# Optimization experiments

Hardware: AMD Instinct MI355X
Metric: run time of the kernel (lower is better)

## Reference

```python
import jax, jax.numpy as jnp
import numpy as np
import math

S, B, D_MODEL = 1024, 2, 1024
N_HEADS = 16
D_HEAD = D_MODEL // N_HEADS
C = 32  # compressed_len


def _xavier(key, shape):
    fan_in, fan_out = shape[-1], shape[-2] if len(shape) > 1 else shape[-1]
    limit = math.sqrt(6.0 / (fan_in + fan_out))
    return jax.random.uniform(key, shape, jnp.float32, -limit, limit)


def setup_inputs() -> dict:
    key = jax.random.key(0)
    ks = jax.random.split(key, 10)
    return {
        "x": jax.random.normal(ks[0], (S, B, D_MODEL), jnp.float32),
        "q_down": _xavier(ks[1], (C, D_MODEL)),
        "Wq": _xavier(ks[2], (D_MODEL, D_MODEL)),
        "bq": jnp.zeros((D_MODEL,), jnp.float32),
        "Wk": _xavier(ks[3], (D_MODEL, D_MODEL)),
        "bk": jnp.zeros((D_MODEL,), jnp.float32),
        "Wv": _xavier(ks[4], (D_MODEL, D_MODEL)),
        "bv": jnp.zeros((D_MODEL,), jnp.float32),
        "Wo": _xavier(ks[5], (D_MODEL, D_MODEL)),
        "bo": jnp.zeros((D_MODEL,), jnp.float32),
    }


def reference(x, q_down, Wq, bq, Wk, bk, Wv, bv, Wo, bo):
    # x: (s, b, d_model); causal=True, rope=None, dropout inactive (eval)
    s, b, d_model = x.shape
    h, dh = N_HEADS, D_HEAD
    scale = 1.0 / math.sqrt(dh)

    q_u = x @ Wq.T + bq                       # (s,b,dm)
    k_d = x @ Wk.T + bk
    v_d = x @ Wv.T + bv
    v_d_k = v_d @ Wk.T + bk
    v_d_v = v_d @ Wv.T + bv

    def heads(t):  # (s,b,dm) -> (b,h,s,dh)
        return t.reshape(s, b, h, dh).transpose(1, 2, 0, 3)

    q_u = heads(q_u) * scale
    k_d = heads(k_d)
    v_d_kv = jnp.concatenate([heads(v_d_k), heads(v_d_v)], axis=-1)  # (b,h,s,2dh)

    q_d = q_down.reshape(C, h, dh).transpose(1, 0, 2) * scale        # (h,c,dh)

    down = jnp.einsum('hcd,bhsd->bhcs', q_d, k_d)                    # (b,h,c,s)
    w = jnp.exp(down - jnp.max(down, axis=-1, keepdims=True))
    norm = jnp.cumsum(w, axis=-1)

    # (b,h,c,s,2dh): running compressed KV state
    kv_u = jnp.cumsum(w[..., None] * v_d_kv[:, :, None, :, :], axis=3) / norm[..., None]
    k_u, v_u = jnp.split(kv_u, 2, axis=-1)                           # each (b,h,c,s,dh)

    up = jnp.einsum('bhsd,bhcsd->bhsc', q_u, k_u)
    up = jax.nn.softmax(up, axis=-1)
    out = jnp.einsum('bhsc,bhcsd->bhsd', up, v_u)                    # (b,h,s,dh)

    out = out.transpose(2, 0, 1, 3).reshape(s, b, d_model)
    return out @ Wo.T + bo
```

## Files before the change

### kernel.cpp

```cpp
#include <hip/hip_runtime.h>
#include <cstdint>
#include <cstddef>

#define S_LEN 1024
#define BATCH 2
#define DM    1024
#define NH    16
#define DH    64
#define CC    32
#define SB    2048
#define TSD   128
#define NCHD  8

using short8 = __attribute__((ext_vector_type(8))) short;
using f32x4  = __attribute__((ext_vector_type(4))) float;

__device__ __forceinline__ float b2f(unsigned short u) {
    union { unsigned int i; float f; } v; v.i = ((unsigned int)u) << 16; return v.f;
}
__device__ __forceinline__ unsigned short f2b(float f) {
    union { float f; unsigned int i; } v; v.f = f;
    unsigned int x = v.i;
    unsigned int r = x + 0x7FFFu + ((x >> 16) & 1u);
    return (unsigned short)(r >> 16);
}

__device__ __forceinline__ void async_ld16(const unsigned short* g, unsigned short* l) {
    __builtin_amdgcn_global_load_lds(
        (const __attribute__((address_space(1))) unsigned int*)g,
        (__attribute__((address_space(3))) unsigned int*)l,
        16, 0, 0);
}

__global__ __launch_bounds__(256) void k_convert(
    const void* x, const void* qd,
    const void* wq, const void* wk, const void* wv, const void* wo,
    const void* bq, const void* bk, const void* bv, const void* bo,
    int* __restrict__ flag,
    unsigned short* xb, unsigned short* qdb,
    unsigned short* Wqb, unsigned short* Wkb, unsigned short* Wvb, unsigned short* Wob,
    float* biasf)
{
    __shared__ int cnt;
    if (threadIdx.x == 0) cnt = 0;
    __syncthreads();
    {
        const unsigned short* xs = (const unsigned short*)x;
        int local = 0;
        for (int i = threadIdx.x; i < 1024; i += 256) {
            unsigned e = (xs[i * 2] >> 7) & 0xFF;
            if (e >= 90 && e <= 160) local++;
        }
        atomicAdd(&cnt, local);
    }
    __syncthreads();
    const int isbf = (cnt >= 640);
    if (blockIdx.x == 0 && threadIdx.x == 0) *flag = isbf;

    const size_t tid = (size_t)blockIdx.x * 256 + threadIdx.x;
    const size_t stride = (size_t)gridDim.x * 256;

    if (!isbf) {
        auto cv = [&](const void* src, unsigned short* dst, size_t n) {
            const float4* s = (const float4*)src;
            for (size_t i = tid; i < n / 4; i += stride) {
                float4 v = s[i];
                ushort4 o;
                o.x = f2b(v.x); o.y = f2b(v.y); o.z = f2b(v.z); o.w = f2b(v.w);
                ((ushort4*)dst)[i] = o;
            }
        };
        cv(x,  xb,  (size_t)SB * DM);
        cv(qd, qdb, (size_t)CC * DM);
        cv(wq, Wqb, (size_t)DM * DM);
        cv(wk, Wkb, (size_t)DM * DM);
        cv(wv, Wvb, (size_t)DM * DM);
        cv(wo, Wob, (size_t)DM * DM);
    }
    for (size_t i = tid; i < 5 * DM; i += stride) {
        int w = (int)(i >> 10), o = (int)(i & 1023);
        float val;
        if (w == 4) val = 0.f;
        else {
            const void* bp = (w == 0) ? bq : ((w == 1) ? bk : ((w == 2) ? bv : bo));
            val = isbf ? b2f(((const unsigned short*)bp)[o]) : ((const float*)bp)[o];
        }
        biasf[i] = val;
    }
}

__global__ __launch_bounds__(256) void k_prep(const unsigned short* __restrict__ Wv0,
                                              const unsigned short* __restrict__ Wv1,
                                              const unsigned short* __restrict__ Wk0,
                                              const unsigned short* __restrict__ Wk1,
                                              const int* __restrict__ flag,
                                              const float* __restrict__ biasf,
                                              unsigned short* __restrict__ WvT,
                                              float* __restrict__ b2k,
                                              float* __restrict__ b2v)
{
    const int isbf = *flag;
    const unsigned short* Wvb = isbf ? Wv1 : Wv0;
    const unsigned short* Wkb = isbf ? Wk1 : Wk0;
    const int t = threadIdx.x;
    if (blockIdx.x < 128) {
        const int r0 = (blockIdx.x & 7) * 128;
        const int c0 = (blockIdx.x >> 3) * 64;
        __shared__ unsigned short T[128 * 68];
        for (int u = t; u < 128 * 8; u += 256) {
            int r = u >> 3, cb = (u & 7) * 8;
            *(short8*)&T[r * 68 + cb] = *(const short8*)&Wvb[(size_t)(r0 + r) * DM + c0 + cb];
        }
        __syncthreads();
        for (int u = t; u < 64 * 16; u += 256) {
            int c = u >> 4, r8 = (u & 15) * 8;
            short8 o;
#pragma unroll
            for (int k = 0; k < 8; ++k) o[k] = T[(r8 + k) * 68 + c];
            *(short8*)&WvT[(size_t)(c0 + c) * DM + r0 + r8] = o;
        }
    } else {
        const int idx = blockIdx.x - 128;
        const int set = idx >> 5;
        const int bx = idx & 31;
        const unsigned short* W = set ? Wvb : Wkb;
        const float* bvf = biasf + 2048;
        const float* badd = set ? (biasf + 2048) : (biasf + 1024);
        float* out = set ? b2v : b2k;
        const int w = t >> 6, l = t & 63;
        const int gw = bx * 4 + w;
        for (int i = 0; i < 8; ++i) {
            int row = gw * 8 + i;
            const unsigned short* wr = &W[(size_t)row * DM + l * 16];
            short8 a = *(const short8*)wr;
            short8 b = *(const short8*)(wr + 8);
            float s = 0.f;
#pragma unroll
            for (int j = 0; j < 8; ++j) {
                s += b2f((unsigned short)a[j]) * bvf[l * 16 + j];
                s += b2f((unsigned short)b[j]) * bvf[l * 16 + 8 + j];
            }
#pragma unroll
            for (int m = 1; m < 64; m <<= 1) s += __shfl_xor(s, m);
            if (l == 0) out[row] = s + badd[row];
        }
    }
}

struct GArg {
    const unsigned short* A0;
    const unsigned short* A1;
    const unsigned short* B0;
    const unsigned short* B1;
    const float* bias;
    void* out;
    float scale;
    int mode;
};

__global__ __launch_bounds__(256) void gemm_bt(GArg g0, GArg g1, GArg g2, GArg g3,
                                               const int* __restrict__ flag,
                                               int M, int N, int K)
{
    GArg ga = (blockIdx.z == 0) ? g0 : (blockIdx.z == 1) ? g1 : (blockIdx.z == 2) ? g2 : g3;
    const int isbf = *flag;
    const unsigned short* Ap = isbf ? ga.A1 : ga.A0;
    const unsigned short* Bp = isbf ? ga.B1 : ga.B0;
    const int m0 = blockIdx.y * 128;
    const int n0 = blockIdx.x * 128;
    __shared__ __align__(16) unsigned short As[2][128 * 32];
    __shared__ __align__(16) unsigned short Bs[2][128 * 32];
    const int t = threadIdx.x;
    const int w = t >> 6, l = t & 63;
    const int wy = w >> 1, wx = w & 1;
    const int lr = l >> 2;
    const int lk = (l & 3) * 8;
    const int ln = l & 15;
    const int lq = l >> 4;

    f32x4 acc[4][4] = {};

    const unsigned short* Ab0 = Ap + (size_t)(m0 + w * 32 +      lr) * K + lk;
    const unsigned short* Ab1 = Ap + (size_t)(m0 + w * 32 + 16 + lr) * K + lk;
    const unsigned short* Bb0 = Bp + (size_t)(n0 + w * 32 +      lr) * K + lk;
    const unsigned short* Bb1 = Bp + (size_t)(n0 + w * 32 + 16 + lr) * K + lk;

    for (int kk = 0; kk < K; kk += 64) {
#pragma unroll
        for (int hh = 0; hh < 2; ++hh) {
            async_ld16(Ab0 + kk + hh * 32, &As[hh][w * 1024]);
            async_ld16(Ab1 + kk + hh * 32, &As[hh][w * 1024 + 512]);
            async_ld16(Bb0 + kk + hh * 32, &Bs[hh][w * 1024]);
            async_ld16(Bb1 + kk + hh * 32, &Bs[hh][w * 1024 + 512]);
        }
        __syncthreads();
#pragma unroll
        for (int hh = 0; hh < 2; ++hh) {
            short8 af[4], bfr[4];
#pragma unroll
            for (int i = 0; i < 4; ++i)
                af[i] = *(const short8*)&As[hh][(wy * 64 + i * 16 + ln) * 32 + lq * 8];
#pragma unroll
            for (int j = 0; j < 4; ++j)
                bfr[j] = *(const short8*)&Bs[hh][(wx * 64 + j * 16 + ln) * 32 + lq * 8];
#pragma unroll
            for (int i = 0; i < 4; ++i)
#pragma unroll
                for (int j = 0; j < 4; ++j)
                    acc[i][j] = __builtin_amdgcn_mfma_f32_16x16x32_bf16(af[i], bfr[j], acc[i][j], 0, 0, 0);
        }
        __syncthreads();
    }

    const int f32o = (ga.mode == 0) ? 1 : (ga.mode == 1) ? 0 : (!isbf);
    const float sc = ga.scale;
#pragma unroll
    for (int j = 0; j < 4; ++j) {
        int col = n0 + wx * 64 + j * 16 + ln;
        float bv = ga.bias[col];
#pragma unroll
        for (int i = 0; i < 4; ++i) {
            int row0 = m0 + wy * 64 + i * 16 + lq * 4;
#pragma unroll
            for (int r = 0; r < 4; ++r) {
                float v = (acc[i][j][r] + bv) * sc;
                size_t idx = (size_t)(row0 + r) * N + col;
                if (f32o) ((float*)ga.out)[idx] = v;
                else      ((unsigned short*)ga.out)[idx] = f2b(v);
            }
        }
    }
}

__global__ __launch_bounds__(256) void gemm_bt_n64(GArg g0, GArg g1,
                                                   const int* __restrict__ flag,
                                                   int M, int N, int K)
{
    GArg ga = (blockIdx.z == 0) ? g0 : g1;
    const int isbf = *flag;
    const unsigned short* Ap = isbf ? ga.A1 : ga.A0;
    const unsigned short* Bp = isbf ? ga.B1 : ga.B0;
    const int m0 = blockIdx.y * 128;
    const int n0 = blockIdx.x * 64;
    __shared__ __align__(16) unsigned short As[2][128 * 32];
    __shared__ __align__(16) unsigned short Bs[2][64 * 32];
    const int t = threadIdx.x;
    const int w = t >> 6, l = t & 63;
    const int wy = w >> 1, wx = w & 1;
    const int lr = l >> 2;
    const int lk = (l & 3) * 8;
    const int ln = l & 15;
    const int lq = l >> 4;

    f32x4 acc[4][2] = {};

    const unsigned short* Ab0 = Ap + (size_t)(m0 + w * 32 +      lr) * K + lk;
    const unsigned short* Ab1 = Ap + (size_t)(m0 + w * 32 + 16 + lr) * K + lk;
    const unsigned short* Bb  = Bp + (size_t)(n0 + w * 16 + lr) * K + lk;

    for (int kk = 0; kk < K; kk += 64) {
#pragma unroll
        for (int hh = 0; hh < 2; ++hh) {
            async_ld16(Ab0 + kk + hh * 32, &As[hh][w * 1024]);
            async_ld16(Ab1 + kk + hh * 32, &As[hh][w * 1024 + 512]);
            async_ld16(Bb  + kk + hh * 32, &Bs[hh][w * 512]);
        }
        __syncthreads();
#pragma unroll
        for (int hh = 0; hh < 2; ++hh) {
            short8 af[4], bfr[2];
#pragma unroll
            for (int i = 0; i < 4; ++i)
                af[i] = *(const short8*)&As[hh][(wy * 64 + i * 16 + ln) * 32 + lq * 8];
#pragma unroll
            for (int j = 0; j < 2; ++j)
                bfr[j] = *(const short8*)&Bs[hh][(wx * 32 + j * 16 + ln) * 32 + lq * 8];
#pragma unroll
            for (int i = 0; i < 4; ++i)
#pragma unroll
                for (int j = 0; j < 2; ++j)
                    acc[i][j] = __builtin_amdgcn_mfma_f32_16x16x32_bf16(af[i], bfr[j], acc[i][j], 0, 0, 0);
        }
        __syncthreads();
    }

    const int f32o = (ga.mode == 0) ? 1 : (ga.mode == 1) ? 0 : (!isbf);
    const float sc = ga.scale;
#pragma unroll
    for (int j = 0; j < 2; ++j) {
        int col = n0 + wx * 32 + j * 16 + ln;
        float bv = ga.bias[col];
#pragma unroll
        for (int i = 0; i < 4; ++i) {
            int row0 = m0 + wy * 64 + i * 16 + lq * 4;
#pragma unroll
            for (int r = 0; r < 4; ++r) {
                float v = (acc[i][j][r] + bv) * sc;
                size_t idx = (size_t)(row0 + r) * N + col;
                if (f32o) ((float*)ga.out)[idx] = v;
                else      ((unsigned short*)ga.out)[idx] = f2b(v);
            }
        }
    }
}

__global__ __launch_bounds__(256) void k_down(const unsigned short* __restrict__ kd,
                                              const unsigned short* __restrict__ qd0,
                                              const unsigned short* __restrict__ qd1,
                                              const int* __restrict__ flag,
                                              float* __restrict__ wbuf,
                                              float* __restrict__ cmax,
                                              float* __restrict__ csum)
{
    const unsigned short* qdw = (*flag) ? qd1 : qd0;
    const int bh = blockIdx.x;
    const int b = bh >> 4, h = bh & 15;
    const int chunk = blockIdx.y;
    const int s0 = chunk * TSD;
    const int t = threadIdx.x;
    const int w = t >> 6, l = t & 63;
    const int ln = l & 15, lq = l >> 4;

    __shared__ __align__(16) unsigned short QD[32 * 72];
    __shared__ __align__(16) unsigned short KT[128 * 72];
    __shared__ float SS[32 * 132];
    __shared__ float pm[256];
    __shared__ float cmf[CC];

    {
        int r = t >> 3, cb = (t & 7) * 8;
        *(short8*)&QD[r * 72 + cb] = *(const short8*)&qdw[(size_t)r * DM + h * DH + cb];
    }
    for (int u = t; u < 128 * 8; u += 256) {
        int r = u >> 3, cb = (u & 7) * 8;
        *(short8*)&KT[r * 72 + cb] =
            *(const short8*)&kd[(size_t)((s0 + r) * BATCH + b) * DM + h * DH + cb];
    }
    __syncthreads();

    f32x4 accG[2][2] = {};
#pragma unroll
    for (int ks = 0; ks < 2; ++ks) {
        short8 a8[2], b8[2];
#pragma unroll
        for (int i = 0; i < 2; ++i)
            a8[i] = *(const short8*)&QD[(i * 16 + ln) * 72 + ks * 32 + lq * 8];
#pragma unroll
        for (int j = 0; j < 2; ++j)
            b8[j] = *(const short8*)&KT[(w * 32 + j * 16 + ln) * 72 + ks * 32 + lq * 8];
#pragma unroll
        for (int i = 0; i < 2; ++i)
#pragma unroll
            for (int j = 0; j < 2; ++j)
                accG[i][j] = __builtin_amdgcn_mfma_f32_16x16x32_bf16(a8[i], b8[j], accG[i][j], 0, 0, 0);
    }
#pragma unroll
    for (int i = 0; i < 2; ++i) {
#pragma unroll
        for (int j = 0; j < 2; ++j) {
            int sl = w * 32 + j * 16 + ln;
#pragma unroll
            for (int r = 0; r < 4; ++r) {
                int c = i * 16 + lq * 4 + r;
                float v = accG[i][j][r] * 0.125f;
                SS[c * 132 + sl] = v;
                wbuf[((size_t)bh * CC + c) * S_LEN + s0 + sl] = v;
            }
        }
    }
    __syncthreads();

    const int c = t >> 3, sub = t & 7;
    float lmax = -3.4e38f;
#pragma unroll
    for (int k = 0; k < 16; ++k) lmax = fmaxf(lmax, SS[c * 132 + sub * 16 + k]);
    lmax = fmaxf(lmax, __shfl_xor(lmax, 1));
    lmax = fmaxf(lmax, __shfl_xor(lmax, 2));
    lmax = fmaxf(lmax, __shfl_xor(lmax, 4));
    if (sub == 0) {
        cmf[c] = lmax;
        cmax[((size_t)bh * CC + c) * NCHD + chunk] = lmax;
    }
    __syncthreads();
    const float cm = cmf[c];
    float es = 0.f;
#pragma unroll
    for (int k = 0; k < 16; ++k) es += __expf(SS[c * 132 + sub * 16 + k] - cm);
    es += __shfl_xor(es, 1);
    es += __shfl_xor(es, 2);
    es += __shfl_xor(es, 4);
    if (sub == 0) csum[((size_t)bh * CC + c) * NCHD + chunk] = es;
}

__global__ __launch_bounds__(256) void k_wapply(const float* __restrict__ wbuf,
                                                const float* __restrict__ cmax,
                                                const float* __restrict__ csum,
                                                unsigned short* __restrict__ wb,
                                                unsigned short* __restrict__ wT,
                                                float* __restrict__ invn)
{
    const int bh = blockIdx.x, seg = blockIdx.y;
    const int t = threadIdx.x;
    __shared__ float gm[CC];
    __shared__ float basep[CC];
    __shared__ float psum[CC][9];
    __shared__ unsigned short wTt[128 * 40];
    __shared__ float invt[128 * 36];

    if (t < CC) {
        const size_t cb = (size_t)(bh * CC + t) * NCHD;
        float m = cmax[cb];
#pragma unroll
        for (int g = 1; g < NCHD; ++g) m = fmaxf(m, cmax[cb + g]);
        gm[t] = m;
        float bsum = 0.f;
        for (int k = 0; k < seg; ++k)
            bsum += csum[cb + k] * __expf(cmax[cb + k] - m);
        basep[t] = bsum;
    }
    __syncthreads();

    const int c = t >> 3, sub = t & 7;
    const float gmc = gm[c];
    const size_t rbase = (size_t)bh * 32768 + c * 1024 + seg * 128 + sub * 16;
    float w16[16];
    float s = 0.f;
#pragma unroll
    for (int i = 0; i < 16; ++i) {
        float v = __expf(wbuf[rbase + i] - gmc);
        w16[i] = v; s += v;
    }
    psum[c][sub] = s;
    short8 o0, o1;
#pragma unroll
    for (int i = 0; i < 8; ++i) { o0[i] = f2b(w16[i]); o1[i] = f2b(w16[8 + i]); }
    *(short8*)&wb[rbase] = o0;
    *(short8*)&wb[rbase + 8] = o1;
#pragma unroll
    for (int i = 0; i < 16; ++i) wTt[(sub * 16 + i) * 40 + c] = f2b(w16[i]);
    __syncthreads();

    float run = basep[c];
    for (int k = 0; k < sub; ++k) run += psum[c][k];
#pragma unroll
    for (int i = 0; i < 16; ++i) {
        run += w16[i];
        invt[(sub * 16 + i) * 36 + c] = 1.0f / fmaxf(run, 1e-30f);
    }
    __syncthreads();

    for (int u = t; u < 128 * 4; u += 256) {
        int r = u >> 2, cb = (u & 3) * 8;
        *(short8*)&wT[(size_t)bh * 32768 + (seg * 128 + r) * 32 + cb] =
            *(const short8*)&wTt[r * 40 + cb];
    }
    for (int u = t; u < 128 * 8; u += 256) {
        int r = u >> 3, cb = (u & 7) * 4;
        *(float4*)&invn[(size_t)bh * 32768 + (seg * 128 + r) * 32 + cb] =
            *(const float4*)&invt[r * 36 + cb];
    }
}

__global__ __launch_bounds__(256) void k_state(const unsigned short* __restrict__ wb,
                                               const unsigned short* __restrict__ vdk,
                                               const unsigned short* __restrict__ vdv,
                                               float* __restrict__ Mst,
                                               float* __restrict__ NTst)
{
    const int bh = blockIdx.x, ch = blockIdx.y;
    const int b = bh >> 4, h = bh & 15;
    const int s0 = ch * 64;
    const int t = threadIdx.x;
    const int w = t >> 6, l = t & 63;
    const int ln = l & 15, lq = l >> 4;
    __shared__ __align__(16) unsigned short Ws[32 * 72];
    __shared__ __align__(16) unsigned short T1[64 * 72];
    __shared__ __align__(16) unsigned short T2[64 * 72];
    __shared__ __align__(16) unsigned short KT[64 * 72];
    __shared__ __align__(16) unsigned short VT[64 * 72];

    for (int u = t; u < 32 * 8; u += 256) {
        int r = u >> 3, cb = (u & 7) * 8;
        *(short8*)&Ws[r * 72 + cb] = *(const short8*)&wb[(size_t)bh * 32768 + r * 1024 + s0 + cb];
    }
    for (int u = t; u < 64 * 8; u += 256) {
        int r = u >> 3, cb = (u & 7) * 8;
        *(short8*)&T1[r * 72 + cb] =
            *(const short8*)&vdk[(size_t)((s0 + r) * BATCH + b) * DM + h * DH + cb];
        *(short8*)&T2[r * 72 + cb] =
            *(const short8*)&vdv[(size_t)((s0 + r) * BATCH + b) * DM + h * DH + cb];
    }
    __syncthreads();
    for (int u = t; u < 64 * 8; u += 256) {
        int d = u >> 3, s8 = (u & 7) * 8;
        short8 o1, o2;
#pragma unroll
        for (int k = 0; k < 8; ++k) {
            o1[k] = T1[(s8 + k) * 72 + d];
            o2[k] = T2[(s8 + k) * 72 + d];
        }
        *(short8*)&KT[d * 72 + s8] = o1;
        *(short8*)&VT[d * 72 + s8] = o2;
    }
    __syncthreads();

    f32x4 accM[2] = {};
#pragma unroll
    for (int ks = 0; ks < 2; ++ks) {
        short8 b8 = *(const short8*)&KT[(w * 16 + ln) * 72 + ks * 32 + lq * 8];
#pragma unroll
        for (int i = 0; i < 2; ++i) {
            short8 a8 = *(const short8*)&Ws[(i * 16 + ln) * 72 + ks * 32 + lq * 8];
            accM[i] = __builtin_amdgcn_mfma_f32_16x16x32_bf16(a8, b8, accM[i], 0, 0, 0);
        }
    }
#pragma unroll
    for (int i = 0; i < 2; ++i)
#pragma unroll
        for (int r = 0; r < 4; ++r)
            Mst[((size_t)(bh * 16 + ch) * 32 + i * 16 + lq * 4 + r) * 64 + w * 16 + ln] = accM[i][r];

    f32x4 accN[2] = {};
#pragma unroll
    for (int ks = 0; ks < 2; ++ks) {
        short8 a8 = *(const short8*)&VT[(w * 16 + ln) * 72 + ks * 32 + lq * 8];
#pragma unroll
        for (int j = 0; j < 2; ++j) {
            short8 b8 = *(const short8*)&Ws[(j * 16 + ln) * 72 + ks * 32 + lq * 8];
            accN[j] = __builtin_amdgcn_mfma_f32_16x16x32_bf16(a8, b8, accN[j], 0, 0, 0);
        }
    }
#pragma unroll
    for (int j = 0; j < 2; ++j)
#pragma unroll
        for (int r = 0; r < 4; ++r)
            NTst[((size_t)(bh * 16 + ch) * 64 + w * 16 + lq * 4 + r) * 32 + j * 16 + ln] = accN[j][r];
}

__global__ __launch_bounds__(256) void k_prefix(const float* __restrict__ Mst,
                                                const float* __restrict__ NTst,
                                                unsigned short* __restrict__ Mcum,
                                                unsigned short* __restrict__ NTcum)
{
    const int bh = blockIdx.x;
    const float* src = blockIdx.y ? NTst : Mst;
    unsigned short* dst = blockIdx.y ? NTcum : Mcum;
    const int e0 = threadIdx.x * 8;
    float run[8];
#pragma unroll
    for (int j = 0; j < 8; ++j) run[j] = 0.f;
    for (int ch = 0; ch < 16; ++ch) {
        size_t off = (size_t)(bh * 16 + ch) * 2048 + e0;
        short8 ob;
#pragma unroll
        for (int j = 0; j < 8; ++j) ob[j] = f2b(run[j]);
        *(short8*)&dst[off] = ob;
#pragma unroll
        for (int j = 0; j < 8; ++j) run[j] += src[off + j];
    }
}

__global__ __launch_bounds__(256) void k_att(
    const unsigned short* __restrict__ qu,
    const unsigned short* __restrict__ vdk,
    const unsigned short* __restrict__ wb,
    const float* __restrict__ invn,
    const unsigned short* __restrict__ wT,
    const unsigned short* __restrict__ vdv,
    const unsigned short* __restrict__ Mcum,
    const unsigned short* __restrict__ NTcum,
    unsigned short* __restrict__ attout)
{
    const int bh = blockIdx.x, b = bh >> 4, h = bh & 15;
    const int qi = blockIdx.y;
    const int s0 = qi * 64;
    const int t = threadIdx.x;
    const int w = t >> 6, l = t & 63;
    const int wy = w >> 1, wx = w & 1;
    const int ln = l & 15, lq = l >> 4;

    __shared__ __align__(16) unsigned short Qs[64 * 72];
    __shared__ __align__(16) unsigned short Gs[64 * 72];
    __shared__ __align__(16) unsigned short Kd[64 * 72];
    __shared__ __align__(16) unsigned short Wd[32 * 72];
    __shared__ __align__(16) unsigned short WTd[64 * 40];
    __shared__ __align__(16) unsigned short VTd[64 * 72];
    __shared__ __align__(16) unsigned short Mc[32 * 72];
    __shared__ __align__(16) unsigned short Nc[64 * 40];

    for (int u = t; u < 64 * 8; u += 256) {
        int r = u >> 3, cb = (u & 7) * 8;
        *(short8*)&Qs[r * 72 + cb] =
            *(const short8*)&qu[(size_t)(s0 + r) * 2048 + b * 1024 + h * 64 + cb];
        *(short8*)&Kd[r * 72 + cb] =
            *(const short8*)&vdk[(size_t)(s0 + r) * 2048 + b * 1024 + h * 64 + cb];
        *(short8*)&Gs[r * 72 + cb] =
            *(const short8*)&vdv[(size_t)(s0 + r) * 2048 + b * 1024 + h * 64 + cb];
    }
    for (int u = t; u < 32 * 8; u += 256) {
        int r = u >> 3, cb = (u & 7) * 8;
        *(short8*)&Wd[r * 72 + cb] =
            *(const short8*)&wb[(size_t)bh * 32768 + r * 1024 + s0 + cb];
        *(short8*)&Mc[r * 72 + cb] =
            *(const short8*)&Mcum[((size_t)(bh * 16 + qi) * 32 + r) * 64 + cb];
    }
    for (int u = t; u < 64 * 4; u += 256) {
        int r = u >> 2, cb = (u & 3) * 8;
        *(short8*)&WTd[r * 40 + cb] =
            *(const short8*)&wT[(size_t)bh * 32768 + (s0 + r) * 32 + cb];
        *(short8*)&Nc[r * 40 + cb] =
            *(const short8*)&NTcum[((size_t)(bh * 16 + qi) * 64 + r) * 32 + cb];
    }
    __syncthreads();

    for (int u = t; u < 64 * 8; u += 256) {
        int d = u >> 3, s8 = (u & 7) * 8;
        short8 o;
#pragma unroll
        for (int k = 0; k < 8; ++k) o[k] = Gs[(s8 + k) * 72 + d];
        *(short8*)&VTd[d * 72 + s8] = o;
    }
    __syncthreads();

    {
        f32x4 accG[2][2] = {};
#pragma unroll
        for (int ks = 0; ks < 2; ++ks) {
            short8 a8[2], b8[2];
#pragma unroll
            for (int i = 0; i < 2; ++i)
                a8[i] = *(const short8*)&Qs[(wy * 32 + i * 16 + ln) * 72 + ks * 32 + lq * 8];
#pragma unroll
            for (int j = 0; j < 2; ++j)
                b8[j] = *(const short8*)&Kd[(wx * 32 + j * 16 + ln) * 72 + ks * 32 + lq * 8];
#pragma unroll
            for (int i = 0; i < 2; ++i)
#pragma unroll
                for (int j = 0; j < 2; ++j)
                    accG[i][j] = __builtin_amdgcn_mfma_f32_16x16x32_bf16(a8[i], b8[j], accG[i][j], 0, 0, 0);
        }
        __syncthreads();
#pragma unroll
        for (int i = 0; i < 2; ++i) {
            int row = wy * 32 + i * 16 + lq * 4;
#pragma unroll
            for (int j = 0; j < 2; ++j) {
                int col = wx * 32 + j * 16 + ln;
#pragma unroll
                for (int r = 0; r < 4; ++r) {
                    float v = accG[i][j][r];
                    if (col > row + r) v = 0.f;
                    Gs[(row + r) * 72 + col] = f2b(v);
                }
            }
        }
    }
    __syncthreads();

    f32x4 accU[2] = {};
#pragma unroll
    for (int ks = 0; ks < 2; ++ks) {
        short8 ga = *(const short8*)&Gs[(w * 16 + ln) * 72 + ks * 32 + lq * 8];
        short8 qa = *(const short8*)&Qs[(w * 16 + ln) * 72 + ks * 32 + lq * 8];
#pragma unroll
        for (int j = 0; j < 2; ++j) {
            short8 wf = *(const short8*)&Wd[(j * 16 + ln) * 72 + ks * 32 + lq * 8];
            short8 mf = *(const short8*)&Mc[(j * 16 + ln) * 72 + ks * 32 + lq * 8];
            accU[j] = __builtin_amdgcn_mfma_f32_16x16x32_bf16(ga, wf, accU[j], 0, 0, 0);
            accU[j] = __builtin_amdgcn_mfma_f32_16x16x32_bf16(qa, mf, accU[j], 0, 0, 0);
        }
    }
    __syncthreads();

    {
        int rowl = w * 16 + lq * 4;
#pragma unroll
        for (int r = 0; r < 4; ++r) {
            int srow = s0 + rowl + r;
            float inv0 = invn[(size_t)bh * 32768 + srow * 32 + ln];
            float inv1 = invn[(size_t)bh * 32768 + srow * 32 + 16 + ln];
            float l0 = accU[0][r] * inv0;
            float l1 = accU[1][r] * inv1;
            float m = fmaxf(l0, l1);
#pragma unroll
            for (int msk = 1; msk < 16; msk <<= 1) m = fmaxf(m, __shfl_xor(m, msk));
            float e0 = __expf(l0 - m), e1 = __expf(l1 - m);
            float Z = e0 + e1;
#pragma unroll
            for (int msk = 1; msk < 16; msk <<= 1) Z += __shfl_xor(Z, msk);
            float iz = 1.0f / Z;
            Qs[(rowl + r) * 40 + ln]      = f2b(e0 * iz * inv0);
            Qs[(rowl + r) * 40 + 16 + ln] = f2b(e1 * iz * inv1);
        }
    }
    __syncthreads();

    short8 pa[2];
#pragma unroll
    for (int i = 0; i < 2; ++i)
        pa[i] = *(const short8*)&Qs[(wy * 32 + i * 16 + ln) * 40 + lq * 8];
    {
        f32x4 accS[2][2] = {};
        short8 b8[2];
#pragma unroll
        for (int j = 0; j < 2; ++j)
            b8[j] = *(const short8*)&WTd[(wx * 32 + j * 16 + ln) * 40 + lq * 8];
#pragma unroll
        for (int i = 0; i < 2; ++i)
#pragma unroll
            for (int j = 0; j < 2; ++j)
                accS[i][j] = __builtin_amdgcn_mfma_f32_16x16x32_bf16(pa[i], b8[j], accS[i][j], 0, 0, 0);
#pragma unroll
        for (int i = 0; i < 2; ++i) {
            int row = wy * 32 + i * 16 + lq * 4;
#pragma unroll
            for (int j = 0; j < 2; ++j) {
                int col = wx * 32 + j * 16 + ln;
#pragma unroll
                for (int r = 0; r < 4; ++r) {
                    float v = accS[i][j][r];
                    if (col > row + r) v = 0.f;
                    Gs[(row + r) * 72 + col] = f2b(v);
                }
            }
        }
    }
    __syncthreads();

    {
        f32x4 accO[2][2] = {};
        short8 n8[2];
#pragma unroll
        for (int j = 0; j < 2; ++j)
            n8[j] = *(const short8*)&Nc[(wx * 32 + j * 16 + ln) * 40 + lq * 8];
#pragma unroll
        for (int i = 0; i < 2; ++i)
#pragma unroll
            for (int j = 0; j < 2; ++j)
                accO[i][j] = __builtin_amdgcn_mfma_f32_16x16x32_bf16(pa[i], n8[j], accO[i][j], 0, 0, 0);
#pragma unroll
        for (int ks = 0; ks < 2; ++ks) {
            short8 a8[2], b8[2];
#pragma unroll
            for (int i = 0; i < 2; ++i)
                a8[i] = *(const short8*)&Gs[(wy * 32 + i * 16 + ln) * 72 + ks * 32 + lq * 8];
#pragma unroll
            for (int j = 0; j < 2; ++j)
                b8[j] = *(const short8*)&VTd[(wx * 32 + j * 16 + ln) * 72 + ks * 32 + lq * 8];
#pragma unroll
            for (int i = 0; i < 2; ++i)
#pragma unroll
                for (int j = 0; j < 2; ++j)
                    accO[i][j] = __builtin_amdgcn_mfma_f32_16x16x32_bf16(a8[i], b8[j], accO[i][j], 0, 0, 0);
        }
#pragma unroll
        for (int i = 0; i < 2; ++i) {
            int rowb = s0 + wy * 32 + i * 16 + lq * 4;
#pragma unroll
            for (int j = 0; j < 2; ++j) {
                int d = wx * 32 + j * 16 + ln;
#pragma unroll
                for (int r = 0; r < 4; ++r)
                    attout[(size_t)(rowb + r) * 2048 + b * 1024 + h * 64 + d] = f2b(accO[i][j][r]);
            }
        }
    }
}

extern "C" void kernel_launch(void* const* d_in, const int* in_sizes, int n_in,
                              void* d_out, int out_size, void* d_ws, size_t ws_size,
                              hipStream_t stream)
{
    (void)in_sizes; (void)n_in; (void)out_size; (void)ws_size;
    char* ws = (char*)d_ws;
    const size_t MB = (size_t)1 << 20;
    const size_t KB = (size_t)1 << 10;
    unsigned short* attout = (unsigned short*)(ws + 0 * MB);
    unsigned short* q_u    = (unsigned short*)(ws + 4 * MB);
    unsigned short* k_d    = (unsigned short*)(ws + 8 * MB);
    unsigned short* v_dk   = (unsigned short*)(ws + 12 * MB);
    unsigned short* v_dv   = (unsigned short*)(ws + 16 * MB);
    float* wbuf = (float*)(ws + 20 * MB);
    unsigned short* wb  = (unsigned short*)(ws + 24 * MB);
    unsigned short* wT  = (unsigned short*)(ws + 26 * MB);
    float* invn = (float*)(ws + 28 * MB);
    float* Mst  = (float*)(ws + 32 * MB);
    float* NTst = (float*)(ws + 36 * MB);
    unsigned short* Mcum  = (unsigned short*)(ws + 40 * MB);
    unsigned short* NTcum = (unsigned short*)(ws + 42 * MB);
    unsigned short* xb  = (unsigned short*)(ws + 44 * MB);
    unsigned short* Wqb = (unsigned short*)(ws + 48 * MB);
    unsigned short* Wkb = (unsigned short*)(ws + 50 * MB);
    unsigned short* Wvb = (unsigned short*)(ws + 52 * MB);
    unsigned short* Wob = (unsigned short*)(ws + 54 * MB);
    unsigned short* WvT = (unsigned short*)(ws + 56 * MB);
    unsigned short* W2k = (unsigned short*)(ws + 58 * MB);
    unsigned short* W2v = (unsigned short*)(ws + 60 * MB);
    unsigned short* qdb = (unsigned short*)(ws + 62 * MB);
    float* biasf  = (float*)(ws + 62 * MB + 64 * KB);
    float* b2k    = (float*)(ws + 62 * MB + 128 * KB);
    float* b2v    = (float*)(ws + 62 * MB + 132 * KB);
    float* cmax   = (float*)(ws + 62 * MB + 192 * KB);
    float* csum   = (float*)(ws + 62 * MB + 256 * KB);
    int*   flag   = (int*)  (ws + 62 * MB + 320 * KB);

    const unsigned short* xraw  = (const unsigned short*)d_in[0];
    const unsigned short* qdraw = (const unsigned short*)d_in[1];
    const unsigned short* wqraw = (const unsigned short*)d_in[2];
    const unsigned short* wkraw = (const unsigned short*)d_in[4];
    const unsigned short* wvraw = (const unsigned short*)d_in[6];
    const unsigned short* woraw = (const unsigned short*)d_in[8];

    k_convert<<<1024, 256, 0, stream>>>(
        d_in[0], d_in[1], d_in[2], d_in[4], d_in[6], d_in[8],
        d_in[3], d_in[5], d_in[7], d_in[9],
        flag, xb, qdb, Wqb, Wkb, Wvb, Wob, biasf);

    const float* bqf = biasf;
    const float* bkf = biasf + 1024;
    const float* bof = biasf + 3072;
    const float* zerof = biasf + 4096;

    k_prep<<<192, 256, 0, stream>>>(Wvb, wvraw, Wkb, wkraw, flag, biasf, WvT, b2k, b2v);
    GArg wpk{ Wkb, wkraw, WvT, WvT, zerof, (void*)W2k, 1.0f, 1 };
    GArg wpv{ Wvb, wvraw, WvT, WvT, zerof, (void*)W2v, 1.0f, 1 };
    gemm_bt_n64<<<dim3(16, 8, 2), 256, 0, stream>>>(wpk, wpv, flag, DM, DM, DM);

    GArg gq { xb, xraw, Wqb, wqraw, bqf, (void*)q_u, 0.125f, 1 };
    GArg gk { xb, xraw, Wkb, wkraw, bkf, (void*)k_d, 1.0f, 1 };
    GArg gvk{ xb, xraw, W2k, W2k,   b2k, (void*)v_dk, 1.0f, 1 };
    GArg gvv{ xb, xraw, W2v, W2v,   b2v, (void*)v_dv, 1.0f, 1 };
    gemm_bt<<<dim3(8, 16, 4), 256, 0, stream>>>(gq, gk, gvk, gvv, flag, SB, DM, DM);

    k_down<<<dim3(32, NCHD), 256, 0, stream>>>(k_d, qdb, qdraw, flag, wbuf, cmax, csum);
    k_wapply<<<dim3(32, 8), 256, 0, stream>>>(wbuf, cmax, csum, wb, wT, invn);
    k_state<<<dim3(32, 16), 256, 0, stream>>>(wb, v_dk, v_dv, Mst, NTst);
    k_prefix<<<dim3(32, 2), 256, 0, stream>>>(Mst, NTst, Mcum, NTcum);
    k_att<<<dim3(32, 16), 256, 0, stream>>>(q_u, v_dk, wb, invn, wT, v_dv, Mcum, NTcum, attout);

    GArg go{ attout, attout, Wob, woraw, bof, d_out, 1.0f, 2 };
    gemm_bt_n64<<<dim3(16, 16, 1), 256, 0, stream>>>(go, go, flag, SB, DM, DM);
}
```

Measured before the change: 188.9 us.

## Fuse weight-apply and chunk-state kernels; transpose weights in attention kernel instead

Merges k_wapply and k_state into one kernel, k_wstate. It keeps the exponentiated weights in shared memory and computes the per-chunk M/NT state by looping over two 64-row chunks for both the K and V inputs. The separate global wT transposed-weight buffer is removed, and k_att now builds the transpose from the Wd tile it already loads into shared memory. This saves one launch and a global write/read round trip. In exchange, the fused kernel has half as many blocks and processes its four chunk passes serially, which may reduce parallelism.

```diff
diff --git a/kernel.cpp b/kernel.cpp
--- a/kernel.cpp
+++ b/kernel.cpp
@@ -324,7 +324,6 @@
     __shared__ __align__(16) unsigned short QD[32 * 72];
     __shared__ __align__(16) unsigned short KT[128 * 72];
     __shared__ float SS[32 * 132];
-    __shared__ float pm[256];
     __shared__ float cmf[CC];
 
     {
@@ -392,20 +391,29 @@
     if (sub == 0) csum[((size_t)bh * CC + c) * NCHD + chunk] = es;
 }
 
-__global__ __launch_bounds__(256) void k_wapply(const float* __restrict__ wbuf,
+__global__ __launch_bounds__(256) void k_wstate(const float* __restrict__ wbuf,
                                                 const float* __restrict__ cmax,
                                                 const float* __restrict__ csum,
+                                                const unsigned short* __restrict__ vdk,
+                                                const unsigned short* __restrict__ vdv,
                                                 unsigned short* __restrict__ wb,
-                                                unsigned short* __restrict__ wT,
-                                                float* __restrict__ invn)
+                                                float* __restrict__ invn,
+                                                float* __restrict__ Mst,
+                                                float* __restrict__ NTst)
 {
     const int bh = blockIdx.x, seg = blockIdx.y;
+    const int b = bh >> 4, h = bh & 15;
     const int t = threadIdx.x;
+    const int w = t >> 6, l = t & 63;
+    const int ln = l & 15, lq = l >> 4;
+
     __shared__ float gm[CC];
     __shared__ float basep[CC];
     __shared__ float psum[CC][9];
-    __shared__ unsigned short wTt[128 * 40];
+    __shared__ __align__(16) unsigned short Ws[32 * 136];
     __shared__ float invt[128 * 36];
+    __shared__ __align__(16) unsigned short T[64 * 72];
+    __shared__ __align__(16) unsigned short TT[64 * 72];
 
     if (t < CC) {
         const size_t cb = (size_t)(bh * CC + t) * NCHD;
@@ -437,7 +445,7 @@
     *(short8*)&wb[rbase] = o0;
     *(short8*)&wb[rbase + 8] = o1;
 #pragma unroll
-    for (int i = 0; i < 16; ++i) wTt[(sub * 16 + i) * 40 + c] = f2b(w16[i]);
+    for (int i = 0; i < 16; ++i) Ws[c * 136 + sub * 16 + i] = f2b(w16[i]);
     __syncthreads();
 
     float run = basep[c];
@@ -449,92 +457,66 @@
     }
     __syncthreads();
 
-    for (int u = t; u < 128 * 4; u += 256) {
-        int r = u >> 2, cb = (u & 3) * 8;
-        *(short8*)&wT[(size_t)bh * 32768 + (seg * 128 + r) * 32 + cb] =
-            *(const short8*)&wTt[r * 40 + cb];
-    }
     for (int u = t; u < 128 * 8; u += 256) {
         int r = u >> 3, cb = (u & 7) * 4;
         *(float4*)&invn[(size_t)bh * 32768 + (seg * 128 + r) * 32 + cb] =
             *(const float4*)&invt[r * 36 + cb];
     }
-}
-
-__global__ __launch_bounds__(256) void k_state(const unsigned short* __restrict__ wb,
-                                               const unsigned short* __restrict__ vdk,
-                                               const unsigned short* __restrict__ vdv,
-                                               float* __restrict__ Mst,
-                                               float* __restrict__ NTst)
-{
-    const int bh = blockIdx.x, ch = blockIdx.y;
-    const int b = bh >> 4, h = bh & 15;
-    const int s0 = ch * 64;
-    const int t = threadIdx.x;
-    const int w = t >> 6, l = t & 63;
-    const int ln = l & 15, lq = l >> 4;
-    __shared__ __align__(16) unsigned short Ws[32 * 72];
-    __shared__ __align__(16) unsigned short T1[64 * 72];
-    __shared__ __align__(16) unsigned short T2[64 * 72];
-    __shared__ __align__(16) unsigned short KT[64 * 72];
-    __shared__ __align__(16) unsigned short VT[64 * 72];
-
-    for (int u = t; u < 32 * 8; u += 256) {
-        int r = u >> 3, cb = (u & 7) * 8;
-        *(short8*)&Ws[r * 72 + cb] = *(const short8*)&wb[(size_t)bh * 32768 + r * 1024 + s0 + cb];
-    }
-    for (int u = t; u < 64 * 8; u += 256) {
-        int r = u >> 3, cb = (u & 7) * 8;
-        *(short8*)&T1[r * 72 + cb] =
-            *(const short8*)&vdk[(size_t)((s0 + r) * BATCH + b) * DM + h * DH + cb];
-        *(short8*)&T2[r * 72 + cb] =
-            *(const short8*)&vdv[(size_t)((s0 + r) * BATCH + b) * DM + h * DH + cb];
-    }
-    __syncthreads();
-    for (int u = t; u < 64 * 8; u += 256) {
-        int d = u >> 3, s8 = (u & 7) * 8;
-        short8 o1, o2;
-#pragma unroll
-        for (int k = 0; k < 8; ++k) {
-            o1[k] = T1[(s8 + k) * 72 + d];
-            o2[k] = T2[(s8 + k) * 72 + d];
-        }
-        *(short8*)&KT[d * 72 + s8] = o1;
-        *(short8*)&VT[d * 72 + s8] = o2;
-    }
-    __syncthreads();
-
-    f32x4 accM[2] = {};
-#pragma unroll
-    for (int ks = 0; ks < 2; ++ks) {
-        short8 b8 = *(const short8*)&KT[(w * 16 + ln) * 72 + ks * 32 + lq * 8];
-#pragma unroll
-        for (int i = 0; i < 2; ++i) {
-            short8 a8 = *(const short8*)&Ws[(i * 16 + ln) * 72 + ks * 32 + lq * 8];
-            accM[i] = __builtin_amdgcn_mfma_f32_16x16x32_bf16(a8, b8, accM[i], 0, 0, 0);
-        }
-    }
-#pragma unroll
-    for (int i = 0; i < 2; ++i)
-#pragma unroll
-        for (int r = 0; r < 4; ++r)
-            Mst[((size_t)(bh * 16 + ch) * 32 + i * 16 + lq * 4 + r) * 64 + w * 16 + ln] = accM[i][r];
-
-    f32x4 accN[2] = {};
-#pragma unroll
-    for (int ks = 0; ks < 2; ++ks) {
-        short8 a8 = *(const short8*)&VT[(w * 16 + ln) * 72 + ks * 32 + lq * 8];
-#pragma unroll
-        for (int j = 0; j < 2; ++j) {
-            short8 b8 = *(const short8*)&Ws[(j * 16 + ln) * 72 + ks * 32 + lq * 8];
-            accN[j] = __builtin_amdgcn_mfma_f32_16x16x32_bf16(a8, b8, accN[j], 0, 0, 0);
-        }
-    }
-#pragma unroll
-    for (int j = 0; j < 2; ++j)
-#pragma unroll
-        for (int r = 0; r < 4; ++r)
-            NTst[((size_t)(bh * 16 + ch) * 64 + w * 16 + lq * 4 + r) * 32 + j * 16 + ln] = accN[j][r];
+
+    for (int it = 0; it < 4; ++it) {
+        const int ch2 = it >> 1;
+        const int isv = it & 1;
+        const int ch = seg * 2 + ch2;
+        const int s0 = ch * 64;
+        const unsigned short* src = isv ? vdv : vdk;
+        for (int u = t; u < 64 * 8; u += 256) {
+            int r = u >> 3, cb = (u & 7) * 8;
+            *(short8*)&T[r * 72 + cb] =
+                *(const short8*)&src[(size_t)((s0 + r) * BATCH + b) * DM + h * DH + cb];
+        }
+        __syncthreads();
+        for (int u = t; u < 64 * 8; u += 256) {
+            int d = u >> 3, s8 = (u & 7) * 8;
+            short8 o;
+#pragma unroll
+            for (int k = 0; k < 8; ++k) o[k] = T[(s8 + k) * 72 + d];
+            *(short8*)&TT[d * 72 + s8] = o;
+        }
+        __syncthreads();
+        if (!isv) {
+            f32x4 accM[2] = {};
+#pragma unroll
+            for (int ks = 0; ks < 2; ++ks) {
+                short8 b8 = *(const short8*)&TT[(w * 16 + ln) * 72 + ks * 32 + lq * 8];
+#pragma unroll
+                for (int i = 0; i < 2; ++i) {
+                    short8 a8 = *(const short8*)&Ws[(i * 16 + ln) * 136 + ch2 * 64 + ks * 32 + lq * 8];
+                    accM[i] = __builtin_amdgcn_mfma_f32_16x16x32_bf16(a8, b8, accM[i], 0, 0, 0);
+                }
+            }
+#pragma unroll
+            for (int i = 0; i < 2; ++i)
+#pragma unroll
+                for (int r = 0; r < 4; ++r)
+                    Mst[((size_t)(bh * 16 + ch) * 32 + i * 16 + lq * 4 + r) * 64 + w * 16 + ln] = accM[i][r];
+        } else {
+            f32x4 accN[2] = {};
+#pragma unroll
+            for (int ks = 0; ks < 2; ++ks) {
+                short8 a8 = *(const short8*)&TT[(w * 16 + ln) * 72 + ks * 32 + lq * 8];
+#pragma unroll
+                for (int j = 0; j < 2; ++j) {
+                    short8 b8 = *(const short8*)&Ws[(j * 16 + ln) * 136 + ch2 * 64 + ks * 32 + lq * 8];
+                    accN[j] = __builtin_amdgcn_mfma_f32_16x16x32_bf16(a8, b8, accN[j], 0, 0, 0);
+                }
+            }
+#pragma unroll
+            for (int j = 0; j < 2; ++j)
+#pragma unroll
+                for (int r = 0; r < 4; ++r)
+                    NTst[((size_t)(bh * 16 + ch) * 64 + w * 16 + lq * 4 + r) * 32 + j * 16 + ln] = accN[j][r];
+        }
+    }
 }
 
 __global__ __launch_bounds__(256) void k_prefix(const float* __restrict__ Mst,
@@ -565,7 +547,6 @@
     const unsigned short* __restrict__ vdk,
     const unsigned short* __restrict__ wb,
     const float* __restrict__ invn,
-    const unsigned short* __restrict__ wT,
     const unsigned short* __restrict__ vdv,
     const unsigned short* __restrict__ Mcum,
     const unsigned short* __restrict__ NTcum,
@@ -606,8 +587,6 @@
     }
     for (int u = t; u < 64 * 4; u += 256) {
         int r = u >> 2, cb = (u & 3) * 8;
-        *(short8*)&WTd[r * 40 + cb] =
-            *(const short8*)&wT[(size_t)bh * 32768 + (s0 + r) * 32 + cb];
         *(short8*)&Nc[r * 40 + cb] =
             *(const short8*)&NTcum[((size_t)(bh * 16 + qi) * 64 + r) * 32 + cb];
     }
@@ -619,6 +598,13 @@
 #pragma unroll
         for (int k = 0; k < 8; ++k) o[k] = Gs[(s8 + k) * 72 + d];
         *(short8*)&VTd[d * 72 + s8] = o;
+    }
+    for (int u = t; u < 64 * 4; u += 256) {
+        int s = u >> 2, c8 = (u & 3) * 8;
+        short8 o;
+#pragma unroll
+        for (int k = 0; k < 8; ++k) o[k] = Wd[(c8 + k) * 72 + s];
+        *(short8*)&WTd[s * 40 + c8] = o;
     }
     __syncthreads();
 
@@ -782,7 +768,6 @@
     unsigned short* v_dv   = (unsigned short*)(ws + 16 * MB);
     float* wbuf = (float*)(ws + 20 * MB);
     unsigned short* wb  = (unsigned short*)(ws + 24 * MB);
-    unsigned short* wT  = (unsigned short*)(ws + 26 * MB);
     float* invn = (float*)(ws + 28 * MB);
     float* Mst  = (float*)(ws + 32 * MB);
     float* NTst = (float*)(ws + 36 * MB);
@@ -833,10 +818,9 @@
     gemm_bt<<<dim3(8, 16, 4), 256, 0, stream>>>(gq, gk, gvk, gvv, flag, SB, DM, DM);
 
     k_down<<<dim3(32, NCHD), 256, 0, stream>>>(k_d, qdb, qdraw, flag, wbuf, cmax, csum);
-    k_wapply<<<dim3(32, 8), 256, 0, stream>>>(wbuf, cmax, csum, wb, wT, invn);
-    k_state<<<dim3(32, 16), 256, 0, stream>>>(wb, v_dk, v_dv, Mst, NTst);
+    k_wstate<<<dim3(32, 8), 256, 0, stream>>>(wbuf, cmax, csum, v_dk, v_dv, wb, invn, Mst, NTst);
     k_prefix<<<dim3(32, 2), 256, 0, stream>>>(Mst, NTst, Mcum, NTcum);
-    k_att<<<dim3(32, 16), 256, 0, stream>>>(q_u, v_dk, wb, invn, wT, v_dv, Mcum, NTcum, attout);
+    k_att<<<dim3(32, 16), 256, 0, stream>>>(q_u, v_dk, wb, invn, v_dv, Mcum, NTcum, attout);
 
     GArg go{ attout, attout, Wob, woraw, bof, d_out, 1.0f, 2 };
     gemm_bt_n64<<<dim3(16, 16, 1), 256, 0, stream>>>(go, go, flag, SB, DM, DM);
```

After: 189.1 us. No clear change (+0.1%).
